# Kernel optimization log

Measured on AMD Instinct MI355X. Metric: run time of the kernel, lower is better.

Reference implementation:

```python
import jax, jax.numpy as jnp
import numpy as np

SEQ_LEN, KEY_DIM, VAL_DIM, NUM_FEATURES, BATCH = 2048, 512, 512, 1024, 8


def setup_inputs() -> dict:
    key = jax.random.key(0)
    ks = jax.random.split(key, 7)
    x = jax.random.normal(ks[0], (BATCH, SEQ_LEN, NUM_FEATURES), dtype=jnp.float32)
    s = 1.0 / np.sqrt(NUM_FEATURES)
    Wq = jax.random.normal(ks[1], (NUM_FEATURES, KEY_DIM), dtype=jnp.float32) * s
    bq = jnp.zeros((KEY_DIM,), dtype=jnp.float32)
    Wk = jax.random.normal(ks[2], (NUM_FEATURES, KEY_DIM), dtype=jnp.float32) * s
    bk = jnp.zeros((KEY_DIM,), dtype=jnp.float32)
    Wv = jax.random.normal(ks[3], (NUM_FEATURES, VAL_DIM), dtype=jnp.float32) * s
    bv = jnp.zeros((VAL_DIM,), dtype=jnp.float32)
    return {"x": x, "Wq": Wq, "bq": bq, "Wk": Wk, "bk": bk, "Wv": Wv, "bv": bv}


def reference(x, Wq, bq, Wk, bk, Wv, bv):
    # x: [B, S, F]
    S = x.shape[1]
    q = x @ Wq + bq                      # [B, S, K]
    k = x @ Wk + bk                      # [B, S, K]
    v = x @ Wv + bv                      # [B, S, V]
    logits = jnp.einsum('bqd,bkd->bqk', q, k) / jnp.sqrt(jnp.float32(KEY_DIM))
    # additive causal mask: -inf above diagonal
    causal = jnp.tril(jnp.ones((S, S), dtype=bool))
    logits = jnp.where(causal, logits, -jnp.inf)
    probs = jax.nn.softmax(logits, axis=-1)
    read = jnp.einsum('bqk,bkv->bqv', probs, v)  # [B, S, V]
    return jnp.concatenate([x, read], axis=-1)   # [B, S, F+V]
```

## Files before the change

### kernel.cpp

```cpp
#include <hip/hip_runtime.h>

#define BB 8
#define SS 2048
#define FF 1024
#define DD 512

typedef __attribute__((ext_vector_type(4))) float f32x4;
typedef __attribute__((ext_vector_type(8))) short s16x8;
typedef __attribute__((ext_vector_type(4))) short s16x4;

__device__ __forceinline__ unsigned short f2bf(float f) {
  unsigned int u = __builtin_bit_cast(unsigned int, f);
  unsigned int r = ((u >> 16) & 1u) + 0x7fffu;
  return (unsigned short)((u + r) >> 16);
}

__device__ __forceinline__ void async16(const void* g, void* l) {
  __builtin_amdgcn_global_load_lds((const __attribute__((address_space(1))) void*)g,
                                   (__attribute__((address_space(3))) void*)l, 16, 0, 0);
}

__global__ __launch_bounds__(256) void convert_x(const float* __restrict__ x,
                                                 float* __restrict__ out,
                                                 unsigned short* __restrict__ xb) {
  size_t idx = ((size_t)blockIdx.x * 256 + threadIdx.x) * 4;
  f32x4 v = *(const f32x4*)(x + idx);
  size_t row = idx >> 10;
  size_t col = idx & 1023;
  *(f32x4*)(out + row * 1536 + col) = v;
  s16x4 h;
  h[0] = (short)f2bf(v[0]); h[1] = (short)f2bf(v[1]);
  h[2] = (short)f2bf(v[2]); h[3] = (short)f2bf(v[3]);
  *(s16x4*)(xb + idx) = h;
}

__global__ __launch_bounds__(256) void prep_w(const float* __restrict__ Wq,
                                              const float* __restrict__ Wk,
                                              const float* __restrict__ Wv,
                                              unsigned short* __restrict__ wt) {
  int z = blockIdx.z;
  const float* W = (z == 0) ? Wq : ((z == 1) ? Wk : Wv);
  unsigned short* o = wt + (size_t)z * DD * FF;
  __shared__ __align__(16) float t[32][33];
  int k0 = blockIdx.x * 32, n0 = blockIdx.y * 32;
  int tid = threadIdx.x;
  int r = tid >> 3, c4 = (tid & 7) * 4;
  f32x4 v = *(const f32x4*)(W + (size_t)(k0 + r) * DD + n0 + c4);
  t[r][c4 + 0] = v[0]; t[r][c4 + 1] = v[1]; t[r][c4 + 2] = v[2]; t[r][c4 + 3] = v[3];
  __syncthreads();
  s16x4 h;
  h[0] = (short)f2bf(t[c4 + 0][r]);
  h[1] = (short)f2bf(t[c4 + 1][r]);
  h[2] = (short)f2bf(t[c4 + 2][r]);
  h[3] = (short)f2bf(t[c4 + 3][r]);
  *(s16x4*)(o + (size_t)(n0 + r) * FF + k0 + c4) = h;
}

__global__ __launch_bounds__(256, 2) void gemm_qkv(
    const unsigned short* __restrict__ xb, const unsigned short* __restrict__ wt,
    const float* __restrict__ bq, const float* __restrict__ bk, const float* __restrict__ bv,
    unsigned short* __restrict__ qo, unsigned short* __restrict__ ko,
    unsigned short* __restrict__ vto) {
  const int wsel = blockIdx.z;
  const unsigned short* W = wt + (size_t)wsel * DD * FF;
  const float* bias = (wsel == 0) ? bq : ((wsel == 1) ? bk : bv);
  const int m0 = blockIdx.x * 128, n0 = blockIdx.y * 128;

  __shared__ __align__(16) char smem[36864];
  unsigned short* Al = (unsigned short*)smem;
  unsigned short* Bl = (unsigned short*)(smem + 8192);

  const int tid = threadIdx.x;
  const int lane = tid & 63, wv = tid >> 6;
  const int wr = wv >> 1, wc = wv & 1;
  const int l15 = lane & 15, lg = lane >> 4;

  const f32x4 fzero = {0.f, 0.f, 0.f, 0.f};
  f32x4 acc[4][4];
#pragma unroll
  for (int i = 0; i < 4; ++i)
#pragma unroll
    for (int j = 0; j < 4; ++j) acc[i][j] = fzero;

  for (int k0 = 0; k0 < FF; k0 += 32) {
#pragma unroll
    for (int is = 0; is < 2; ++is) {
      int chunk = (is * 4 + wv) * 64;
      int lin = (chunk + lane) * 8;
      int r = lin >> 5, c = lin & 31;
      async16(xb + (size_t)(m0 + r) * FF + k0 + c, (char*)Al + (size_t)chunk * 16);
      async16(W + (size_t)(n0 + r) * FF + k0 + c, (char*)Bl + (size_t)chunk * 16);
    }
    __syncthreads();
    s16x8 af[4], bf[4];
#pragma unroll
    for (int mi = 0; mi < 4; ++mi)
      af[mi] = *(const s16x8*)(&Al[(wr * 64 + mi * 16 + l15) * 32 + lg * 8]);
#pragma unroll
    for (int ni = 0; ni < 4; ++ni)
      bf[ni] = *(const s16x8*)(&Bl[(wc * 64 + ni * 16 + l15) * 32 + lg * 8]);
#pragma unroll
    for (int mi = 0; mi < 4; ++mi)
#pragma unroll
      for (int ni = 0; ni < 4; ++ni)
        acc[mi][ni] = __builtin_amdgcn_mfma_f32_16x16x32_bf16(af[mi], bf[ni], acc[mi][ni], 0, 0, 0);
    __syncthreads();
  }

  const float QS = 0.0637583894f;
  if (wsel == 2) {
    unsigned short* Tw = (unsigned short*)smem + (size_t)wv * 64 * 72;
#pragma unroll
    for (int ni = 0; ni < 4; ++ni) {
      int cl = ni * 16 + l15;
      float bvv = bias[n0 + wc * 64 + cl];
#pragma unroll
      for (int mi = 0; mi < 4; ++mi)
#pragma unroll
        for (int j = 0; j < 4; ++j)
          Tw[cl * 72 + mi * 16 + lg * 4 + j] = f2bf(acc[mi][ni][j] + bvv);
    }
    asm volatile("s_waitcnt lgkmcnt(0)" ::: "memory");
    const int bb = (m0 + wr * 64) >> 11;
    const int sb = (m0 + wr * 64) & 2047;
    const int cb = n0 + wc * 64;
#pragma unroll
    for (int p = 0; p < 8; ++p) {
      int cl = p * 8 + (lane >> 3);
      int sl = (lane & 7) * 8;
      s16x8 vv = *(const s16x8*)(Tw + cl * 72 + sl);
      *(s16x8*)(vto + ((size_t)(bb * DD + cb + cl)) * SS + sb + sl) = vv;
    }
  } else {
    unsigned short* o = wsel ? ko : qo;
#pragma unroll
    for (int ni = 0; ni < 4; ++ni) {
      int cg = n0 + wc * 64 + ni * 16 + l15;
      float bvv = bias[cg];
#pragma unroll
      for (int mi = 0; mi < 4; ++mi) {
#pragma unroll
        for (int j = 0; j < 4; ++j) {
          int rg = m0 + wr * 64 + mi * 16 + lg * 4 + j;
          float val = acc[mi][ni][j] + bvv;
          if (wsel == 0) val *= QS;
          o[(size_t)rg * DD + cg] = f2bf(val);
        }
      }
    }
  }
}

__global__ __launch_bounds__(256, 2) void attn(const unsigned short* __restrict__ qg,
                                               const unsigned short* __restrict__ kgl,
                                               const unsigned short* __restrict__ vtg,
                                               float* __restrict__ out) {
  const int b = blockIdx.y;
  const int vhalf = blockIdx.z;
  const int qt = (vhalf == 0) ? blockIdx.x : (31 - blockIdx.x);
  const int q0 = qt * 64;

  __shared__ __align__(16) unsigned short Kl[32 * 520];
  __shared__ __align__(16) unsigned short Vl[256 * 40];
  __shared__ __align__(16) unsigned short Pl[4 * 16 * 40];

  const int tid = threadIdx.x;
  const int lane = tid & 63, w = tid >> 6;
  const int l15 = lane & 15, lg = lane >> 4;

  const int kR = tid >> 6, kC = (tid & 63) * 8;
  const int vN = tid >> 2, vC = (tid & 3) * 8;
  const unsigned short* kbase = kgl + ((size_t)(b * SS + kR)) * DD + kC;
  const unsigned short* vbase = vtg + ((size_t)(b * DD + vhalf * 256 + vN)) * SS + vC;

  s16x8 qf[16];
  {
    const unsigned short* qp = qg + ((size_t)(b * SS + q0 + w * 16 + l15)) * DD + lg * 8;
#pragma unroll
    for (int kk = 0; kk < 16; ++kk) qf[kk] = *(const s16x8*)(qp + kk * 32);
  }

  const f32x4 fzero = {0.f, 0.f, 0.f, 0.f};
  f32x4 oacc[16];
#pragma unroll
  for (int n = 0; n < 16; ++n) oacc[n] = fzero;
  float mrun[4], lsum[4];
#pragma unroll
  for (int i = 0; i < 4; ++i) { mrun[i] = -__builtin_inff(); lsum[i] = 0.f; }

  const int nt = qt * 2 + 2;

  f32x4 kreg[8], vreg[4];
#pragma unroll
  for (int it = 0; it < 8; ++it)
    kreg[it] = *(const f32x4*)(kbase + (size_t)(it * 4) * DD);
#pragma unroll
  for (int it = 0; it < 4; ++it)
    vreg[it] = *(const f32x4*)(vbase + (size_t)(it * 64) * SS);

  for (int t = 0; t < nt; ++t) {
    const int kv0 = t * 32;
    __syncthreads();
#pragma unroll
    for (int it = 0; it < 8; ++it)
      *(f32x4*)(&Kl[(kR + it * 4) * 520 + kC]) = kreg[it];
#pragma unroll
    for (int it = 0; it < 4; ++it)
      *(f32x4*)(&Vl[(vN + it * 64) * 40 + vC]) = vreg[it];
    __syncthreads();

    if (t + 1 < nt) {
      const int nkv = kv0 + 32;
#pragma unroll
      for (int it = 0; it < 8; ++it)
        kreg[it] = *(const f32x4*)(kbase + (size_t)(nkv + it * 4) * DD);
#pragma unroll
      for (int it = 0; it < 4; ++it)
        vreg[it] = *(const f32x4*)(vbase + (size_t)(it * 64) * SS + nkv);
    }

    f32x4 s0 = fzero, s1 = fzero;
#pragma unroll
    for (int kk = 0; kk < 16; ++kk) {
      s16x8 b0 = *(const s16x8*)(&Kl[l15 * 520 + kk * 32 + lg * 8]);
      s16x8 b1 = *(const s16x8*)(&Kl[(16 + l15) * 520 + kk * 32 + lg * 8]);
      s0 = __builtin_amdgcn_mfma_f32_16x16x32_bf16(qf[kk], b0, s0, 0, 0, 0);
      s1 = __builtin_amdgcn_mfma_f32_16x16x32_bf16(qf[kk], b1, s1, 0, 0, 0);
    }

    const int rowb = q0 + w * 16 + lg * 4;
    if (kv0 + 31 > q0 + w * 16) {
#pragma unroll
      for (int i = 0; i < 4; ++i) {
        int rg = rowb + i;
        if (kv0 + l15 > rg)      s0[i] = -__builtin_inff();
        if (kv0 + 16 + l15 > rg) s1[i] = -__builtin_inff();
      }
    }

    float corr[4];
#pragma unroll
    for (int i = 0; i < 4; ++i) {
      float tm = fmaxf(s0[i], s1[i]);
      tm = fmaxf(tm, __shfl_xor(tm, 1));
      tm = fmaxf(tm, __shfl_xor(tm, 2));
      tm = fmaxf(tm, __shfl_xor(tm, 4));
      tm = fmaxf(tm, __shfl_xor(tm, 8));
      float mo = mrun[i];
      float mn = fmaxf(mo, tm);
      mrun[i] = mn;
      float c = __builtin_amdgcn_exp2f(mo - mn);
      float p0 = __builtin_amdgcn_exp2f(s0[i] - mn);
      float p1 = __builtin_amdgcn_exp2f(s1[i] - mn);
      lsum[i] = lsum[i] * c + p0 + p1;
      corr[i] = c;
      Pl[w * 640 + (lg * 4 + i) * 40 + l15] = f2bf(p0);
      Pl[w * 640 + (lg * 4 + i) * 40 + 16 + l15] = f2bf(p1);
    }

#pragma unroll
    for (int n = 0; n < 16; ++n) {
      oacc[n][0] *= corr[0]; oacc[n][1] *= corr[1];
      oacc[n][2] *= corr[2]; oacc[n][3] *= corr[3];
    }

    asm volatile("s_waitcnt lgkmcnt(0)" ::: "memory");
    s16x8 pa = *(const s16x8*)(&Pl[w * 640 + l15 * 40 + lg * 8]);
#pragma unroll
    for (int n = 0; n < 16; ++n) {
      s16x8 vv = *(const s16x8*)(&Vl[(n * 16 + l15) * 40 + lg * 8]);
      oacc[n] = __builtin_amdgcn_mfma_f32_16x16x32_bf16(pa, vv, oacc[n], 0, 0, 0);
    }
  }

  float inv[4];
#pragma unroll
  for (int i = 0; i < 4; ++i) {
    float rs = lsum[i];
    rs += __shfl_xor(rs, 1);
    rs += __shfl_xor(rs, 2);
    rs += __shfl_xor(rs, 4);
    rs += __shfl_xor(rs, 8);
    inv[i] = 1.0f / rs;
  }
  size_t obase = ((size_t)(b * SS + q0 + w * 16 + lg * 4)) * 1536 + 1024 + vhalf * 256;
#pragma unroll
  for (int n = 0; n < 16; ++n) {
#pragma unroll
    for (int i = 0; i < 4; ++i) {
      out[obase + (size_t)i * 1536 + n * 16 + l15] = oacc[n][i] * inv[i];
    }
  }
}

extern "C" void kernel_launch(void* const* d_in, const int* in_sizes, int n_in,
                              void* d_out, int out_size, void* d_ws, size_t ws_size,
                              hipStream_t stream) {
  (void)in_sizes; (void)n_in; (void)out_size; (void)ws_size;
  const float* x  = (const float*)d_in[0];
  const float* Wq = (const float*)d_in[1];
  const float* bq = (const float*)d_in[2];
  const float* Wk = (const float*)d_in[3];
  const float* bk = (const float*)d_in[4];
  const float* Wv = (const float*)d_in[5];
  const float* bv = (const float*)d_in[6];
  float* out = (float*)d_out;

  char* ws = (char*)d_ws;
  unsigned short* xb  = (unsigned short*)(ws);
  unsigned short* wt  = (unsigned short*)(ws + 33554432);
  unsigned short* qw  = (unsigned short*)(ws + 33554432 + 3145728);
  unsigned short* kw  = qw + (size_t)16384 * 512;
  unsigned short* vtw = kw + (size_t)16384 * 512;

  convert_x<<<16384, 256, 0, stream>>>(x, out, xb);
  prep_w<<<dim3(32, 16, 3), 256, 0, stream>>>(Wq, Wk, Wv, wt);
  gemm_qkv<<<dim3(128, 4, 3), 256, 0, stream>>>(xb, wt, bq, bk, bv, qw, kw, vtw);
  attn<<<dim3(32, 8, 2), 256, 0, stream>>>(qw, kw, vtw, out);
}
```

Baseline: 377.4 us.

## Swizzle attention LDS, remap GEMM blocks per XCD, lazy softmax rescale, raise occupancy

The attention kernel replaces padded K/V shared-memory rows with XOR-swizzled unpadded layouts, which cuts LDS footprint while aiming to keep bank conflicts low. The online softmax now rescales only when the running max grows by more than a threshold, and skips the accumulator rescale when no lane in the wave needs it. The QKV GEMM uses a 1D grid remapped so the blocks on each XCD share M-tiles, improving L2 reuse. Both kernels ask for 3 waves per SIMD in launch bounds. The lazy rescale trades exactness of the max for fewer multiplies and relies on bounded exponent growth, and the higher occupancy target may force register spills.

```diff
diff --git a/kernel.cpp b/kernel.cpp
--- a/kernel.cpp
+++ b/kernel.cpp
@@ -56,15 +56,21 @@
   *(s16x4*)(o + (size_t)(n0 + r) * FF + k0 + c4) = h;
 }
 
-__global__ __launch_bounds__(256, 2) void gemm_qkv(
+__global__ __launch_bounds__(256, 3) void gemm_qkv(
     const unsigned short* __restrict__ xb, const unsigned short* __restrict__ wt,
     const float* __restrict__ bq, const float* __restrict__ bk, const float* __restrict__ bv,
     unsigned short* __restrict__ qo, unsigned short* __restrict__ ko,
     unsigned short* __restrict__ vto) {
-  const int wsel = blockIdx.z;
+  const int orig = blockIdx.x;
+  const int wg = (orig & 7) * 192 + (orig >> 3);
+  const int mt = wg / 12;
+  const int r12 = wg - mt * 12;
+  const int n0 = (r12 & 3) * 128;
+  const int wsel = r12 >> 2;
+  const int m0 = mt * 128;
+
   const unsigned short* W = wt + (size_t)wsel * DD * FF;
   const float* bias = (wsel == 0) ? bq : ((wsel == 1) ? bk : bv);
-  const int m0 = blockIdx.x * 128, n0 = blockIdx.y * 128;
 
   __shared__ __align__(16) char smem[36864];
   unsigned short* Al = (unsigned short*)smem;
@@ -151,7 +157,7 @@
   }
 }
 
-__global__ __launch_bounds__(256, 2) void attn(const unsigned short* __restrict__ qg,
+__global__ __launch_bounds__(256, 3) void attn(const unsigned short* __restrict__ qg,
                                                const unsigned short* __restrict__ kgl,
                                                const unsigned short* __restrict__ vtg,
                                                float* __restrict__ out) {
@@ -160,8 +166,8 @@
   const int qt = (vhalf == 0) ? blockIdx.x : (31 - blockIdx.x);
   const int q0 = qt * 64;
 
-  __shared__ __align__(16) unsigned short Kl[32 * 520];
-  __shared__ __align__(16) unsigned short Vl[256 * 40];
+  __shared__ __align__(16) unsigned short Kl[32 * 512];
+  __shared__ __align__(16) unsigned short Vl[256 * 32];
   __shared__ __align__(16) unsigned short Pl[4 * 16 * 40];
 
   const int tid = threadIdx.x;
@@ -170,6 +176,7 @@
 
   const int kR = tid >> 6, kC = (tid & 63) * 8;
   const int vN = tid >> 2, vC = (tid & 3) * 8;
+  const int vS = vC ^ (((vN >> 2) & 3) << 3);
   const unsigned short* kbase = kgl + ((size_t)(b * SS + kR)) * DD + kC;
   const unsigned short* vbase = vtg + ((size_t)(b * DD + vhalf * 256 + vN)) * SS + vC;
 
@@ -198,15 +205,20 @@
   for (int it = 0; it < 4; ++it)
     vreg[it] = *(const f32x4*)(vbase + (size_t)(it * 64) * SS);
 
+  const int ksw = (l15 & 7) << 3;
+  const int vsw = ((l15 >> 2) & 3) << 3;
+
   for (int t = 0; t < nt; ++t) {
     const int kv0 = t * 32;
     __syncthreads();
 #pragma unroll
-    for (int it = 0; it < 8; ++it)
-      *(f32x4*)(&Kl[(kR + it * 4) * 520 + kC]) = kreg[it];
+    for (int it = 0; it < 8; ++it) {
+      int row = kR + it * 4;
+      *(f32x4*)(&Kl[row * 512 + (kC ^ ((row & 7) << 3))]) = kreg[it];
+    }
 #pragma unroll
     for (int it = 0; it < 4; ++it)
-      *(f32x4*)(&Vl[(vN + it * 64) * 40 + vC]) = vreg[it];
+      *(f32x4*)(&Vl[(vN + it * 64) * 32 + vS]) = vreg[it];
     __syncthreads();
 
     if (t + 1 < nt) {
@@ -222,8 +234,8 @@
     f32x4 s0 = fzero, s1 = fzero;
 #pragma unroll
     for (int kk = 0; kk < 16; ++kk) {
-      s16x8 b0 = *(const s16x8*)(&Kl[l15 * 520 + kk * 32 + lg * 8]);
-      s16x8 b1 = *(const s16x8*)(&Kl[(16 + l15) * 520 + kk * 32 + lg * 8]);
+      s16x8 b0 = *(const s16x8*)(&Kl[l15 * 512 + ((kk * 32 + lg * 8) ^ ksw)]);
+      s16x8 b1 = *(const s16x8*)(&Kl[(16 + l15) * 512 + ((kk * 32 + lg * 8) ^ ksw)]);
       s0 = __builtin_amdgcn_mfma_f32_16x16x32_bf16(qf[kk], b0, s0, 0, 0, 0);
       s1 = __builtin_amdgcn_mfma_f32_16x16x32_bf16(qf[kk], b1, s1, 0, 0, 0);
     }
@@ -239,6 +251,7 @@
     }
 
     float corr[4];
+    int needr = 0;
 #pragma unroll
     for (int i = 0; i < 4; ++i) {
       float tm = fmaxf(s0[i], s1[i]);
@@ -247,28 +260,32 @@
       tm = fmaxf(tm, __shfl_xor(tm, 4));
       tm = fmaxf(tm, __shfl_xor(tm, 8));
       float mo = mrun[i];
-      float mn = fmaxf(mo, tm);
+      bool upd = (tm > mo + 8.0f);
+      float mn = upd ? tm : mo;
       mrun[i] = mn;
-      float c = __builtin_amdgcn_exp2f(mo - mn);
+      float c = upd ? __builtin_amdgcn_exp2f(mo - mn) : 1.0f;
       float p0 = __builtin_amdgcn_exp2f(s0[i] - mn);
       float p1 = __builtin_amdgcn_exp2f(s1[i] - mn);
       lsum[i] = lsum[i] * c + p0 + p1;
       corr[i] = c;
+      needr |= (int)upd;
       Pl[w * 640 + (lg * 4 + i) * 40 + l15] = f2bf(p0);
       Pl[w * 640 + (lg * 4 + i) * 40 + 16 + l15] = f2bf(p1);
     }
 
-#pragma unroll
-    for (int n = 0; n < 16; ++n) {
-      oacc[n][0] *= corr[0]; oacc[n][1] *= corr[1];
-      oacc[n][2] *= corr[2]; oacc[n][3] *= corr[3];
+    if (__any(needr)) {
+#pragma unroll
+      for (int n = 0; n < 16; ++n) {
+        oacc[n][0] *= corr[0]; oacc[n][1] *= corr[1];
+        oacc[n][2] *= corr[2]; oacc[n][3] *= corr[3];
+      }
     }
 
     asm volatile("s_waitcnt lgkmcnt(0)" ::: "memory");
     s16x8 pa = *(const s16x8*)(&Pl[w * 640 + l15 * 40 + lg * 8]);
 #pragma unroll
     for (int n = 0; n < 16; ++n) {
-      s16x8 vv = *(const s16x8*)(&Vl[(n * 16 + l15) * 40 + lg * 8]);
+      s16x8 vv = *(const s16x8*)(&Vl[(n * 16 + l15) * 32 + (lg * 8 ^ vsw)]);
       oacc[n] = __builtin_amdgcn_mfma_f32_16x16x32_bf16(pa, vv, oacc[n], 0, 0, 0);
     }
   }
@@ -315,6 +332,6 @@
 
   convert_x<<<16384, 256, 0, stream>>>(x, out, xb);
   prep_w<<<dim3(32, 16, 3), 256, 0, stream>>>(Wq, Wk, Wv, wt);
-  gemm_qkv<<<dim3(128, 4, 3), 256, 0, stream>>>(xb, wt, bq, bk, bv, qw, kw, vtw);
+  gemm_qkv<<<1536, 256, 0, stream>>>(xb, wt, bq, bk, bv, qw, kw, vtw);
   attn<<<dim3(32, 8, 2), 256, 0, stream>>>(qw, kw, vtw, out);
 }
```

After: 807.0 us. 114% more time.
